# Kernel optimization log

Hardware: AMD Instinct MI355X
Metric: run time of the kernel (lower is better)

Reference implementation:

```python
import jax, jax.numpy as jnp
import numpy as np

N = 100000      # nodes
E = 3200000     # edges (avg degree 32)
IN_DIM = 256
OUT_DIM = 256


def setup_inputs() -> dict:
    key = jax.random.key(0)
    k1, k2, k3, k4, k5, k6 = jax.random.split(key, 6)
    row = jax.random.randint(k1, (E,), 0, N, dtype=jnp.int32)
    col = jax.random.randint(k2, (E,), 0, N, dtype=jnp.int32)
    vals = jax.random.uniform(k3, (E,), dtype=jnp.float32)
    x = jax.random.normal(k4, (N, IN_DIM), dtype=jnp.float32)
    W = jax.random.normal(k5, (IN_DIM, OUT_DIM), dtype=jnp.float32) * (IN_DIM ** -0.5)
    b = jax.random.normal(k6, (OUT_DIM,), dtype=jnp.float32) * 0.01
    return {"row": row, "col": col, "vals": vals, "x": x, "W": W, "b": b}


def reference(row, col, vals, x, W, b):
    # H = A_hat @ x  (sparse COO matmul via gather + segment-sum scatter)
    gathered = vals[:, None] * x[col]              # [E, in_dim]
    agg = jax.ops.segment_sum(gathered, row, num_segments=N)  # [N, in_dim]
    # Dense linear: agg @ W + b
    return agg @ W + b                             # [N, out_dim]
```

## Files before the change

kernel.cpp:

```cpp
#include <hip/hip_runtime.h>

#define IN_DIM 256
#define OUT_DIM 256
#define NBITS 8
#define CHUNK 8192
#define CAP 13056
#define VAL_SCALE 32767.0f
#define INV_VAL_SCALE (1.0f / 32767.0f)

typedef __attribute__((ext_vector_type(8))) short bf16x8;
typedef __attribute__((ext_vector_type(4))) float f32x4;

static __device__ __forceinline__ unsigned short f2bf(float f) {
    unsigned int u = __float_as_uint(f);
    u = (u + 0x7FFFu + ((u >> 16) & 1u)) >> 16;
    return (unsigned short)u;
}


__global__ void init_cursors(int* __restrict__ cursor, int nb) {
    int i = blockIdx.x * blockDim.x + threadIdx.x;
    if (i < nb) cursor[i] = i * CAP;
}

__global__ __launch_bounds__(512) void bucket_scatter(const int* __restrict__ row,
                                                      const int* __restrict__ col,
                                                      const float* __restrict__ vals,
                                                      int* __restrict__ cursor,
                                                      unsigned int* __restrict__ edge_p,
                                                      unsigned char* __restrict__ rowloc,
                                                      int E, int nb) {
    __shared__ int hist[512];
    __shared__ int gbase[512];
    __shared__ int cur[512];
    const int t = threadIdx.x;
    const int base_e = blockIdx.x * CHUNK;
    for (int i = t; i < nb; i += 512) { hist[i] = 0; cur[i] = 0; }
    __syncthreads();
#pragma unroll
    for (int i = 0; i < CHUNK / 512; ++i) {
        int e = base_e + i * 512 + t;
        if (e < E) atomicAdd(&hist[row[e] >> NBITS], 1);
    }
    __syncthreads();
    for (int i = t; i < nb; i += 512) {
        int c = hist[i];
        if (c > 0) gbase[i] = atomicAdd(&cursor[i], c);
    }
    __syncthreads();
#pragma unroll
    for (int i = 0; i < CHUNK / 512; ++i) {
        int e = base_e + i * 512 + t;
        if (e < E) {
            int r = row[e];
            int bk = r >> NBITS;
            int loc = atomicAdd(&cur[bk], 1);
            int dest = gbase[bk] + loc;
            unsigned int vq = (unsigned int)(vals[e] * VAL_SCALE + 0.5f);
            edge_p[dest] = ((unsigned int)col[e] << 15) | vq;
            rowloc[dest] = (unsigned char)(r & 255);
        }
    }
}

__global__ __launch_bounds__(512) void bucket_to_csr(const int* __restrict__ cursor,
                                                     unsigned int* __restrict__ edge_p,
                                                     const unsigned char* __restrict__ rowloc,
                                                     int2* __restrict__ row_se, int N, int nb) {
    __shared__ unsigned int ep[CAP];
    __shared__ unsigned char rl[CAP];
    __shared__ int cnt[256];
    __shared__ int cur[256];
    __shared__ int fin[256];
    __shared__ int wsum[4];
    const int t = threadIdx.x;
    const int b = blockIdx.x;
    const int gb = b * CAP;
    int m = cursor[b] - gb;
    if (m > CAP) m = CAP;
    if (t < 256) cnt[t] = 0;
    __syncthreads();
    for (int i = t; i < m; i += 512) {
        ep[i] = edge_p[gb + i];
        unsigned char r = rowloc[gb + i];
        rl[i] = r;
        atomicAdd(&cnt[r], 1);
    }
    __syncthreads();
    int v = 0, pcv = 0, incl = 0;
    const int lane = t & 63;
    const int w = t >> 6;
    if (t < 256) {
        v = cnt[t];
        pcv = (v + 7) & ~7;
        incl = pcv;
#pragma unroll
        for (int off = 1; off < 64; off <<= 1) {
            int u = __shfl_up(incl, off, 64);
            if (lane >= off) incl += u;
        }
        if (lane == 63) wsum[w] = incl;
    }
    __syncthreads();
    if (t < 256) {
        int wp = 0;
        for (int k = 0; k < w; ++k) wp += wsum[k];
        int excl = wp + incl - pcv;
        cur[t] = excl;
        fin[t] = excl + pcv;
        const int baseRow = b << NBITS;
        if (t < N - baseRow)
            row_se[baseRow + t] = make_int2(gb + excl, gb + excl + pcv);
    }
    __syncthreads();
    for (int i = t; i < m; i += 512) {
        int r = rl[i];
        int pos = atomicAdd(&cur[r], 1);
        edge_p[gb + pos] = ep[i];
    }
    __syncthreads();
    if (t < 256) {
        for (int pos = cur[t]; pos < fin[t]; ++pos)
            edge_p[gb + pos] = 0u;
    }
}

__global__ __launch_bounds__(256) void convert_W(const float* __restrict__ W,
                                                 unsigned short* __restrict__ Wb) {
    int idx = blockIdx.x * 256 + threadIdx.x;
    int k = idx >> 8, c = idx & 255;
    Wb[(c >> 4) * 4096 + (k >> 3) * 128 + (c & 15) * 8 + (k & 7)] = f2bf(W[idx]);
}

__global__ __launch_bounds__(512) void gemm_y_mfma(const float* __restrict__ x,
                                                   const unsigned short* __restrict__ Wb,
                                                   unsigned short* __restrict__ y, int M) {
    const int t = threadIdx.x;
    const int lane = t & 63;
    const int wid = t >> 6;
    const int wr = wid >> 2;
    const int wc = wid & 3;
    const int blockRow = blockIdx.x * 128;
    const int r0 = blockRow + wr * 64;
    const int c0 = wc * 64;

    f32x4 acc[4][4];
#pragma unroll
    for (int m = 0; m < 4; ++m)
#pragma unroll
        for (int n = 0; n < 4; ++n) acc[m][n] = (f32x4){0.f, 0.f, 0.f, 0.f};

    const int arow_off = lane & 15;
    const int kgrp = lane >> 4;

#pragma unroll
    for (int step = 0; step < 8; ++step) {
        const int k0 = step * 32 + kgrp * 8;
        bf16x8 a[4], bfr[4];
#pragma unroll
        for (int m = 0; m < 4; ++m) {
            int row = r0 + m * 16 + arow_off;
            row = min(row, M - 1);
            const float* xr = x + (size_t)row * IN_DIM + k0;
            float4 f0 = *reinterpret_cast<const float4*>(xr);
            float4 f1 = *reinterpret_cast<const float4*>(xr + 4);
            a[m][0] = (short)f2bf(f0.x); a[m][1] = (short)f2bf(f0.y);
            a[m][2] = (short)f2bf(f0.z); a[m][3] = (short)f2bf(f0.w);
            a[m][4] = (short)f2bf(f1.x); a[m][5] = (short)f2bf(f1.y);
            a[m][6] = (short)f2bf(f1.z); a[m][7] = (short)f2bf(f1.w);
        }
#pragma unroll
        for (int n = 0; n < 4; ++n) {
            int nb = wc * 4 + n;
            bfr[n] = *reinterpret_cast<const bf16x8*>(
                Wb + (size_t)nb * 4096 + (step * 4 + kgrp) * 128 + arow_off * 8);
        }
#pragma unroll
        for (int m = 0; m < 4; ++m)
#pragma unroll
            for (int n = 0; n < 4; ++n)
                acc[m][n] = __builtin_amdgcn_mfma_f32_16x16x32_bf16(a[m], bfr[n], acc[m][n], 0, 0, 0);
    }

#pragma unroll
    for (int m = 0; m < 4; ++m) {
        int rbase = r0 + m * 16 + kgrp * 4;
#pragma unroll
        for (int i = 0; i < 4; ++i) {
            int row = rbase + i;
            if (row < M) {
                unsigned short* yr = y + (size_t)row * OUT_DIM + c0 + arow_off;
#pragma unroll
                for (int n = 0; n < 4; ++n) yr[n * 16] = f2bf(acc[m][n][i]);
            }
        }
    }
}

__global__ __launch_bounds__(256) void aggregate_rows_bf16(const int2* __restrict__ row_se,
                                                           const unsigned int* __restrict__ edge_p,
                                                           const unsigned short* __restrict__ y,
                                                           const float* __restrict__ b,
                                                           float* __restrict__ out, int N) {
    const int lane = threadIdx.x & 63;
    const int w = threadIdx.x >> 6;
    const int r = blockIdx.x * 4 + w;
    if (r >= N) return;

    const int2 se = row_se[r];
    const int start = se.x;
    const int end = se.y;
    const int half = lane >> 5;
    const int d0 = (lane & 31) * 8;

    float acc[8];
#pragma unroll
    for (int i = 0; i < 8; ++i) acc[i] = 0.f;

    for (int j = start; j < end; j += 8) {
        uint4 mp = *reinterpret_cast<const uint4*>(edge_p + j + half * 4);
        float v0 = (float)(mp.x & 0x7fffu) * INV_VAL_SCALE;
        float v1 = (float)(mp.y & 0x7fffu) * INV_VAL_SCALE;
        float v2 = (float)(mp.z & 0x7fffu) * INV_VAL_SCALE;
        float v3 = (float)(mp.w & 0x7fffu) * INV_VAL_SCALE;
        uint4 u0 = *reinterpret_cast<const uint4*>(y + ((size_t)(mp.x >> 15)) * OUT_DIM + d0);
        uint4 u1 = *reinterpret_cast<const uint4*>(y + ((size_t)(mp.y >> 15)) * OUT_DIM + d0);
        uint4 u2 = *reinterpret_cast<const uint4*>(y + ((size_t)(mp.z >> 15)) * OUT_DIM + d0);
        uint4 u3 = *reinterpret_cast<const uint4*>(y + ((size_t)(mp.w >> 15)) * OUT_DIM + d0);
        acc[0] += v0 * __uint_as_float(u0.x << 16);
        acc[1] += v0 * __uint_as_float(u0.x & 0xffff0000u);
        acc[2] += v0 * __uint_as_float(u0.y << 16);
        acc[3] += v0 * __uint_as_float(u0.y & 0xffff0000u);
        acc[4] += v0 * __uint_as_float(u0.z << 16);
        acc[5] += v0 * __uint_as_float(u0.z & 0xffff0000u);
        acc[6] += v0 * __uint_as_float(u0.w << 16);
        acc[7] += v0 * __uint_as_float(u0.w & 0xffff0000u);
        acc[0] += v1 * __uint_as_float(u1.x << 16);
        acc[1] += v1 * __uint_as_float(u1.x & 0xffff0000u);
        acc[2] += v1 * __uint_as_float(u1.y << 16);
        acc[3] += v1 * __uint_as_float(u1.y & 0xffff0000u);
        acc[4] += v1 * __uint_as_float(u1.z << 16);
        acc[5] += v1 * __uint_as_float(u1.z & 0xffff0000u);
        acc[6] += v1 * __uint_as_float(u1.w << 16);
        acc[7] += v1 * __uint_as_float(u1.w & 0xffff0000u);
        acc[0] += v2 * __uint_as_float(u2.x << 16);
        acc[1] += v2 * __uint_as_float(u2.x & 0xffff0000u);
        acc[2] += v2 * __uint_as_float(u2.y << 16);
        acc[3] += v2 * __uint_as_float(u2.y & 0xffff0000u);
        acc[4] += v2 * __uint_as_float(u2.z << 16);
        acc[5] += v2 * __uint_as_float(u2.z & 0xffff0000u);
        acc[6] += v2 * __uint_as_float(u2.w << 16);
        acc[7] += v2 * __uint_as_float(u2.w & 0xffff0000u);
        acc[0] += v3 * __uint_as_float(u3.x << 16);
        acc[1] += v3 * __uint_as_float(u3.x & 0xffff0000u);
        acc[2] += v3 * __uint_as_float(u3.y << 16);
        acc[3] += v3 * __uint_as_float(u3.y & 0xffff0000u);
        acc[4] += v3 * __uint_as_float(u3.z << 16);
        acc[5] += v3 * __uint_as_float(u3.z & 0xffff0000u);
        acc[6] += v3 * __uint_as_float(u3.w << 16);
        acc[7] += v3 * __uint_as_float(u3.w & 0xffff0000u);
    }

#pragma unroll
    for (int i = 0; i < 8; ++i) acc[i] += __shfl_xor(acc[i], 32, 64);

    if (half == 0) {
        float4 b0 = *reinterpret_cast<const float4*>(b + d0);
        float4 b1 = *reinterpret_cast<const float4*>(b + d0 + 4);
        float4 o0 = make_float4(acc[0] + b0.x, acc[1] + b0.y, acc[2] + b0.z, acc[3] + b0.w);
        float4 o1 = make_float4(acc[4] + b1.x, acc[5] + b1.y, acc[6] + b1.z, acc[7] + b1.w);
        float* op = out + (size_t)r * OUT_DIM + d0;
        *reinterpret_cast<float4*>(op) = o0;
        *reinterpret_cast<float4*>(op + 4) = o1;
    }
}

extern "C" void kernel_launch(void* const* d_in, const int* in_sizes, int n_in,
                              void* d_out, int out_size, void* d_ws, size_t ws_size,
                              hipStream_t stream) {
    const int*   row  = (const int*)d_in[0];
    const int*   col  = (const int*)d_in[1];
    const float* vals = (const float*)d_in[2];
    const float* x    = (const float*)d_in[3];
    const float* W    = (const float*)d_in[4];
    const float* b    = (const float*)d_in[5];
    const int E = in_sizes[0];
    const int N = in_sizes[3] / IN_DIM;
    const int nb = (N + 255) >> NBITS;

    float* out = (float*)d_out;

    char* ws = (char*)d_ws;
    size_t off = 0;
    unsigned short* y = (unsigned short*)(ws + off);  off += (size_t)N * OUT_DIM * 2;
    off = (off + 255) & ~(size_t)255;
    unsigned short* Wb = (unsigned short*)(ws + off); off += (size_t)IN_DIM * OUT_DIM * 2;
    off = (off + 255) & ~(size_t)255;
    unsigned int* edge_p = (unsigned int*)(ws + off); off += (size_t)nb * CAP * 4;
    unsigned char* rowloc = (unsigned char*)(ws + off); off += (size_t)nb * CAP;
    off = (off + 255) & ~(size_t)255;
    int* cursor = (int*)(ws + off);                   off += (size_t)nb * 4;
    off = (off + 255) & ~(size_t)255;
    int2* row_se = (int2*)(ws + off);                 off += (size_t)N * 8;

    const int nchunks = (E + CHUNK - 1) / CHUNK;

    convert_W<<<(IN_DIM * OUT_DIM) / 256, 256, 0, stream>>>(W, Wb);
    gemm_y_mfma<<<(N + 127) / 128, 512, 0, stream>>>(x, Wb, y, N);

    init_cursors<<<(nb + 255) / 256, 256, 0, stream>>>(cursor, nb);
    bucket_scatter<<<nchunks, 512, 0, stream>>>(row, col, vals, cursor,
                                                edge_p, rowloc, E, nb);
    bucket_to_csr<<<nb, 512, 0, stream>>>(cursor, edge_p, rowloc, row_se, N, nb);

    aggregate_rows_bf16<<<(N + 3) / 4, 256, 0, stream>>>(row_se, edge_p, y, b, out, N);
}
```

Measured before the change: 444.0 us.

## Fuse GEMM with edge bucket scatter and shrink CSR row padding

Merges the W conversion with cursor initialisation into one prep kernel. Runs the dense MFMA GEMM and the edge bucket scatter as disjoint block ranges of a single launch, so the compute-bound GEMM and the atomic-heavy scatter can overlap on the GPU and fewer kernels are launched. Row padding in the CSR drops from multiples of 8 to multiples of 4, and the aggregation gets a 4-edge tail path, which cuts padded zero-edge gathers. The cost is a larger fused kernel whose register use is set by the GEMM branch, which may lower occupancy for the scatter blocks.

```diff
diff --git a/kernel.cpp b/kernel.cpp
--- a/kernel.cpp
+++ b/kernel.cpp
@@ -17,48 +17,119 @@
     return (unsigned short)u;
 }
 
-
-__global__ void init_cursors(int* __restrict__ cursor, int nb) {
-    int i = blockIdx.x * blockDim.x + threadIdx.x;
-    if (i < nb) cursor[i] = i * CAP;
-}
-
-__global__ __launch_bounds__(512) void bucket_scatter(const int* __restrict__ row,
-                                                      const int* __restrict__ col,
-                                                      const float* __restrict__ vals,
-                                                      int* __restrict__ cursor,
-                                                      unsigned int* __restrict__ edge_p,
-                                                      unsigned char* __restrict__ rowloc,
-                                                      int E, int nb) {
+__global__ __launch_bounds__(256) void prep_kernel(const float* __restrict__ W,
+                                                   unsigned short* __restrict__ Wb,
+                                                   int* __restrict__ cursor, int nb) {
+    int blk = blockIdx.x;
+    int t = threadIdx.x;
+    if (blk < 256) {
+        int idx = blk * 256 + t;
+        int k = idx >> 8, c = idx & 255;
+        Wb[(c >> 4) * 4096 + (k >> 3) * 128 + (c & 15) * 8 + (k & 7)] = f2bf(W[idx]);
+    } else {
+        for (int i = t; i < nb; i += 256) cursor[i] = i * CAP;
+    }
+}
+
+__global__ __launch_bounds__(512) void gemm_scatter_fused(
+        const float* __restrict__ x, const unsigned short* __restrict__ Wb,
+        unsigned short* __restrict__ y, int M,
+        const int* __restrict__ row, const int* __restrict__ col,
+        const float* __restrict__ vals, int* __restrict__ cursor,
+        unsigned int* __restrict__ edge_p, unsigned char* __restrict__ rowloc,
+        int E, int nb, int GB) {
     __shared__ int hist[512];
     __shared__ int gbase[512];
     __shared__ int cur[512];
-    const int t = threadIdx.x;
-    const int base_e = blockIdx.x * CHUNK;
-    for (int i = t; i < nb; i += 512) { hist[i] = 0; cur[i] = 0; }
-    __syncthreads();
-#pragma unroll
-    for (int i = 0; i < CHUNK / 512; ++i) {
-        int e = base_e + i * 512 + t;
-        if (e < E) atomicAdd(&hist[row[e] >> NBITS], 1);
-    }
-    __syncthreads();
-    for (int i = t; i < nb; i += 512) {
-        int c = hist[i];
-        if (c > 0) gbase[i] = atomicAdd(&cursor[i], c);
-    }
-    __syncthreads();
-#pragma unroll
-    for (int i = 0; i < CHUNK / 512; ++i) {
-        int e = base_e + i * 512 + t;
-        if (e < E) {
-            int r = row[e];
-            int bk = r >> NBITS;
-            int loc = atomicAdd(&cur[bk], 1);
-            int dest = gbase[bk] + loc;
-            unsigned int vq = (unsigned int)(vals[e] * VAL_SCALE + 0.5f);
-            edge_p[dest] = ((unsigned int)col[e] << 15) | vq;
-            rowloc[dest] = (unsigned char)(r & 255);
+
+    if (blockIdx.x < (unsigned)GB) {
+        const int t = threadIdx.x;
+        const int lane = t & 63;
+        const int wid = t >> 6;
+        const int wr = wid >> 2;
+        const int wc = wid & 3;
+        const int r0 = blockIdx.x * 128 + wr * 64;
+        const int c0 = wc * 64;
+
+        f32x4 acc[4][4];
+#pragma unroll
+        for (int m = 0; m < 4; ++m)
+#pragma unroll
+            for (int n = 0; n < 4; ++n) acc[m][n] = (f32x4){0.f, 0.f, 0.f, 0.f};
+
+        const int arow_off = lane & 15;
+        const int kgrp = lane >> 4;
+
+#pragma unroll
+        for (int step = 0; step < 8; ++step) {
+            const int k0 = step * 32 + kgrp * 8;
+            bf16x8 a[4], bfr[4];
+#pragma unroll
+            for (int m = 0; m < 4; ++m) {
+                int rr = r0 + m * 16 + arow_off;
+                rr = min(rr, M - 1);
+                const float* xr = x + (size_t)rr * IN_DIM + k0;
+                float4 f0 = *reinterpret_cast<const float4*>(xr);
+                float4 f1 = *reinterpret_cast<const float4*>(xr + 4);
+                a[m][0] = (short)f2bf(f0.x); a[m][1] = (short)f2bf(f0.y);
+                a[m][2] = (short)f2bf(f0.z); a[m][3] = (short)f2bf(f0.w);
+                a[m][4] = (short)f2bf(f1.x); a[m][5] = (short)f2bf(f1.y);
+                a[m][6] = (short)f2bf(f1.z); a[m][7] = (short)f2bf(f1.w);
+            }
+#pragma unroll
+            for (int n = 0; n < 4; ++n) {
+                int nbk = wc * 4 + n;
+                bfr[n] = *reinterpret_cast<const bf16x8*>(
+                    Wb + (size_t)nbk * 4096 + (step * 4 + kgrp) * 128 + arow_off * 8);
+            }
+#pragma unroll
+            for (int m = 0; m < 4; ++m)
+#pragma unroll
+                for (int n = 0; n < 4; ++n)
+                    acc[m][n] = __builtin_amdgcn_mfma_f32_16x16x32_bf16(a[m], bfr[n], acc[m][n], 0, 0, 0);
+        }
+
+#pragma unroll
+        for (int m = 0; m < 4; ++m) {
+            int rbase = r0 + m * 16 + kgrp * 4;
+#pragma unroll
+            for (int i = 0; i < 4; ++i) {
+                int rr = rbase + i;
+                if (rr < M) {
+                    unsigned short* yr = y + (size_t)rr * OUT_DIM + c0 + arow_off;
+#pragma unroll
+                    for (int n = 0; n < 4; ++n) yr[n * 16] = f2bf(acc[m][n][i]);
+                }
+            }
+        }
+    } else {
+        const int t = threadIdx.x;
+        const int base_e = (blockIdx.x - GB) * CHUNK;
+        for (int i = t; i < nb; i += 512) { hist[i] = 0; cur[i] = 0; }
+        __syncthreads();
+#pragma unroll
+        for (int i = 0; i < CHUNK / 512; ++i) {
+            int e = base_e + i * 512 + t;
+            if (e < E) atomicAdd(&hist[row[e] >> NBITS], 1);
+        }
+        __syncthreads();
+        for (int i = t; i < nb; i += 512) {
+            int c = hist[i];
+            if (c > 0) gbase[i] = atomicAdd(&cursor[i], c);
+        }
+        __syncthreads();
+#pragma unroll
+        for (int i = 0; i < CHUNK / 512; ++i) {
+            int e = base_e + i * 512 + t;
+            if (e < E) {
+                int r = row[e];
+                int bk = r >> NBITS;
+                int loc = atomicAdd(&cur[bk], 1);
+                int dest = gbase[bk] + loc;
+                unsigned int vq = (unsigned int)(vals[e] * VAL_SCALE + 0.5f);
+                edge_p[dest] = ((unsigned int)col[e] << 15) | vq;
+                rowloc[dest] = (unsigned char)(r & 255);
+            }
         }
     }
 }
@@ -87,12 +158,11 @@
         atomicAdd(&cnt[r], 1);
     }
     __syncthreads();
-    int v = 0, pcv = 0, incl = 0;
+    int pcv = 0, incl = 0;
     const int lane = t & 63;
     const int w = t >> 6;
     if (t < 256) {
-        v = cnt[t];
-        pcv = (v + 7) & ~7;
+        pcv = (cnt[t] + 3) & ~3;
         incl = pcv;
 #pragma unroll
         for (int off = 1; off < 64; off <<= 1) {
@@ -125,78 +195,6 @@
     }
 }
 
-__global__ __launch_bounds__(256) void convert_W(const float* __restrict__ W,
-                                                 unsigned short* __restrict__ Wb) {
-    int idx = blockIdx.x * 256 + threadIdx.x;
-    int k = idx >> 8, c = idx & 255;
-    Wb[(c >> 4) * 4096 + (k >> 3) * 128 + (c & 15) * 8 + (k & 7)] = f2bf(W[idx]);
-}
-
-__global__ __launch_bounds__(512) void gemm_y_mfma(const float* __restrict__ x,
-                                                   const unsigned short* __restrict__ Wb,
-                                                   unsigned short* __restrict__ y, int M) {
-    const int t = threadIdx.x;
-    const int lane = t & 63;
-    const int wid = t >> 6;
-    const int wr = wid >> 2;
-    const int wc = wid & 3;
-    const int blockRow = blockIdx.x * 128;
-    const int r0 = blockRow + wr * 64;
-    const int c0 = wc * 64;
-
-    f32x4 acc[4][4];
-#pragma unroll
-    for (int m = 0; m < 4; ++m)
-#pragma unroll
-        for (int n = 0; n < 4; ++n) acc[m][n] = (f32x4){0.f, 0.f, 0.f, 0.f};
-
-    const int arow_off = lane & 15;
-    const int kgrp = lane >> 4;
-
-#pragma unroll
-    for (int step = 0; step < 8; ++step) {
-        const int k0 = step * 32 + kgrp * 8;
-        bf16x8 a[4], bfr[4];
-#pragma unroll
-        for (int m = 0; m < 4; ++m) {
-            int row = r0 + m * 16 + arow_off;
-            row = min(row, M - 1);
-            const float* xr = x + (size_t)row * IN_DIM + k0;
-            float4 f0 = *reinterpret_cast<const float4*>(xr);
-            float4 f1 = *reinterpret_cast<const float4*>(xr + 4);
-            a[m][0] = (short)f2bf(f0.x); a[m][1] = (short)f2bf(f0.y);
-            a[m][2] = (short)f2bf(f0.z); a[m][3] = (short)f2bf(f0.w);
-            a[m][4] = (short)f2bf(f1.x); a[m][5] = (short)f2bf(f1.y);
-            a[m][6] = (short)f2bf(f1.z); a[m][7] = (short)f2bf(f1.w);
-        }
-#pragma unroll
-        for (int n = 0; n < 4; ++n) {
-            int nb = wc * 4 + n;
-            bfr[n] = *reinterpret_cast<const bf16x8*>(
-                Wb + (size_t)nb * 4096 + (step * 4 + kgrp) * 128 + arow_off * 8);
-        }
-#pragma unroll
-        for (int m = 0; m < 4; ++m)
-#pragma unroll
-            for (int n = 0; n < 4; ++n)
-                acc[m][n] = __builtin_amdgcn_mfma_f32_16x16x32_bf16(a[m], bfr[n], acc[m][n], 0, 0, 0);
-    }
-
-#pragma unroll
-    for (int m = 0; m < 4; ++m) {
-        int rbase = r0 + m * 16 + kgrp * 4;
-#pragma unroll
-        for (int i = 0; i < 4; ++i) {
-            int row = rbase + i;
-            if (row < M) {
-                unsigned short* yr = y + (size_t)row * OUT_DIM + c0 + arow_off;
-#pragma unroll
-                for (int n = 0; n < 4; ++n) yr[n * 16] = f2bf(acc[m][n][i]);
-            }
-        }
-    }
-}
-
 __global__ __launch_bounds__(256) void aggregate_rows_bf16(const int2* __restrict__ row_se,
                                                            const unsigned int* __restrict__ edge_p,
                                                            const unsigned short* __restrict__ y,
@@ -217,7 +215,8 @@
 #pragma unroll
     for (int i = 0; i < 8; ++i) acc[i] = 0.f;
 
-    for (int j = start; j < end; j += 8) {
+    int j = start;
+    for (; j + 8 <= end; j += 8) {
         uint4 mp = *reinterpret_cast<const uint4*>(edge_p + j + half * 4);
         float v0 = (float)(mp.x & 0x7fffu) * INV_VAL_SCALE;
         float v1 = (float)(mp.y & 0x7fffu) * INV_VAL_SCALE;
@@ -260,6 +259,29 @@
         acc[6] += v3 * __uint_as_float(u3.w << 16);
         acc[7] += v3 * __uint_as_float(u3.w & 0xffff0000u);
     }
+    if (j < end) {
+        uint2 mp = *reinterpret_cast<const uint2*>(edge_p + j + half * 2);
+        float v0 = (float)(mp.x & 0x7fffu) * INV_VAL_SCALE;
+        float v1 = (float)(mp.y & 0x7fffu) * INV_VAL_SCALE;
+        uint4 u0 = *reinterpret_cast<const uint4*>(y + ((size_t)(mp.x >> 15)) * OUT_DIM + d0);
+        uint4 u1 = *reinterpret_cast<const uint4*>(y + ((size_t)(mp.y >> 15)) * OUT_DIM + d0);
+        acc[0] += v0 * __uint_as_float(u0.x << 16);
+        acc[1] += v0 * __uint_as_float(u0.x & 0xffff0000u);
+        acc[2] += v0 * __uint_as_float(u0.y << 16);
+        acc[3] += v0 * __uint_as_float(u0.y & 0xffff0000u);
+        acc[4] += v0 * __uint_as_float(u0.z << 16);
+        acc[5] += v0 * __uint_as_float(u0.z & 0xffff0000u);
+        acc[6] += v0 * __uint_as_float(u0.w << 16);
+        acc[7] += v0 * __uint_as_float(u0.w & 0xffff0000u);
+        acc[0] += v1 * __uint_as_float(u1.x << 16);
+        acc[1] += v1 * __uint_as_float(u1.x & 0xffff0000u);
+        acc[2] += v1 * __uint_as_float(u1.y << 16);
+        acc[3] += v1 * __uint_as_float(u1.y & 0xffff0000u);
+        acc[4] += v1 * __uint_as_float(u1.z << 16);
+        acc[5] += v1 * __uint_as_float(u1.z & 0xffff0000u);
+        acc[6] += v1 * __uint_as_float(u1.w << 16);
+        acc[7] += v1 * __uint_as_float(u1.w & 0xffff0000u);
+    }
 
 #pragma unroll
     for (int i = 0; i < 8; ++i) acc[i] += __shfl_xor(acc[i], 32, 64);
@@ -303,14 +325,15 @@
     off = (off + 255) & ~(size_t)255;
     int2* row_se = (int2*)(ws + off);                 off += (size_t)N * 8;
 
-    const int nchunks = (E + CHUNK - 1) / CHUNK;
-
-    convert_W<<<(IN_DIM * OUT_DIM) / 256, 256, 0, stream>>>(W, Wb);
-    gemm_y_mfma<<<(N + 127) / 128, 512, 0, stream>>>(x, Wb, y, N);
-
-    init_cursors<<<(nb + 255) / 256, 256, 0, stream>>>(cursor, nb);
-    bucket_scatter<<<nchunks, 512, 0, stream>>>(row, col, vals, cursor,
-                                                edge_p, rowloc, E, nb);
+    const int GB = (N + 127) / 128;
+    const int SB = (E + CHUNK - 1) / CHUNK;
+
+    prep_kernel<<<257, 256, 0, stream>>>(W, Wb, cursor, nb);
+
+    gemm_scatter_fused<<<GB + SB, 512, 0, stream>>>(x, Wb, y, N,
+                                                    row, col, vals, cursor,
+                                                    edge_p, rowloc, E, nb, GB);
+
     bucket_to_csr<<<nb, 512, 0, stream>>>(cursor, edge_p, rowloc, row_se, N, nb);
 
     aggregate_rows_bf16<<<(N + 3) / 4, 256, 0, stream>>>(row_se, edge_p, y, b, out, N);
```

New measurement: 410.3 us. -7.6%, faster.
